# Kernel optimization log

Hardware: AMD Instinct MI355X
Metric: run time of the kernel (lower is better)

The kernel has to match this reference:

```python
import jax, jax.numpy as jnp
import numpy as np
import math

N_CLASSES = 1000
CODE_LENGTH = 1024
IN_FEATURES = 4096
BATCH = 512
MAX_PROB = 0.95
POWER = 1.0


def _hadamard(n):
    # Sylvester construction; n must be a power of 2.
    H = np.array([[1.0]], dtype=np.float64)
    while H.shape[0] < n:
        H = np.block([[H, H], [H, -H]])
    return H


def setup_inputs() -> dict:
    key = jax.random.key(0)
    k1, k2, k3 = jax.random.split(key, 3)
    x = jax.random.normal(k1, (BATCH, IN_FEATURES), dtype=jnp.float32)
    out_feat = CODE_LENGTH - 1  # single head: code_length//1 - 1
    # nn.Linear default init: U(-1/sqrt(fan_in), 1/sqrt(fan_in))
    bound = 1.0 / math.sqrt(IN_FEATURES)
    W = jax.random.uniform(k2, (out_feat, IN_FEATURES), dtype=jnp.float32, minval=-bound, maxval=bound)
    b = jax.random.uniform(k3, (out_feat,), dtype=jnp.float32, minval=-bound, maxval=bound)
    labels = jnp.asarray(_hadamard(CODE_LENGTH)[:N_CLASSES, 1:], dtype=jnp.float32)  # (C, L-1)
    eps = jnp.float32(CODE_LENGTH * math.pow((1.0 - MAX_PROB) / (MAX_PROB * (N_CLASSES - 1)), 1.0 / POWER))
    power = jnp.float32(POWER)
    return {"x": x, "W": W, "b": b, "labels": labels, "eps": eps, "power": power}


def reference(x, W, b, labels, eps, power):
    # Linear head: (B, in) @ (in, L-1) + b
    h = jnp.tanh(x @ W.T + b)                               # (B, L-1)
    # L1 distance to each Hadamard code row: (B, 1, L-1) vs (C, L-1)
    d = jnp.sum(jnp.abs(h[:, None, :] - labels), axis=-1)   # (B, C)
    d = jnp.maximum(d, eps)
    inv = 1.0 / jnp.power(d, power)                          # (B, C)
    return inv / jnp.sum(inv, axis=-1, keepdims=True)
```

## Files before the change

### kernel.cpp

```cpp
#include <hip/hip_runtime.h>

#define BATCH 512
#define INFEAT 4096
#define LOUT 1023
#define NCLS 1000
#define NPAD 1024
#define SPLITK 8

typedef __bf16 bf16x8 __attribute__((ext_vector_type(8)));
typedef float f32x4 __attribute__((ext_vector_type(4)));

__device__ __forceinline__ unsigned short f2bf(float a) {
    unsigned u = __builtin_bit_cast(unsigned, a);
    return (unsigned short)((u + 0x7fffu + ((u >> 16) & 1u)) >> 16);
}
__device__ __forceinline__ unsigned f2bf2(float a, float b) {
    return (unsigned)f2bf(a) | ((unsigned)f2bf(b) << 16);
}
__device__ __forceinline__ float bf2f(unsigned short u) {
    return __builtin_bit_cast(float, ((unsigned)u) << 16);
}

__device__ __forceinline__ void gload_lds16(const void* g, void* l) {
    __builtin_amdgcn_global_load_lds(
        (const __attribute__((address_space(1))) void*)g,
        (__attribute__((address_space(3))) void*)l, 16, 0, 0);
}

__global__ __launch_bounds__(256) void k_cvt(const float* __restrict__ x,
                                             const float* __restrict__ W,
                                             unsigned char* __restrict__ xb,
                                             unsigned char* __restrict__ Wb) {
    int blk = blockIdx.x;
    if (blk < 1024) {
        int g = blk * 256 + threadIdx.x;
        int r = g >> 9, k16 = g & 511;
        const float4* p = (const float4*)(x + (size_t)r * INFEAT + k16 * 8);
        float4 v0 = p[0], v1 = p[1];
        uint4 o;
        o.x = f2bf2(v0.x, v0.y); o.y = f2bf2(v0.z, v0.w);
        o.z = f2bf2(v1.x, v1.y); o.w = f2bf2(v1.z, v1.w);
        *(uint4*)(xb + (size_t)r * 8192 + (k16 >> 3) * 128 + (((k16 & 7) ^ (r & 7)) * 16)) = o;
    } else {
        int g = (blk - 1024) * 256 + threadIdx.x;
        int r = g >> 9, k16 = g & 511;
        uint4 o = {0, 0, 0, 0};
        if (r < LOUT) {
            const float4* p = (const float4*)(W + (size_t)r * INFEAT + k16 * 8);
            float4 v0 = p[0], v1 = p[1];
            o.x = f2bf2(v0.x, v0.y); o.y = f2bf2(v0.z, v0.w);
            o.z = f2bf2(v1.x, v1.y); o.w = f2bf2(v1.z, v1.w);
        }
        *(uint4*)(Wb + (size_t)r * 8192 + (k16 >> 3) * 128 + (((k16 & 7) ^ (r & 7)) * 16)) = o;
    }
}

__global__ __launch_bounds__(256, 2) void k_gemm1(
    const unsigned char* __restrict__ xb, const unsigned char* __restrict__ Wb,
    unsigned short* __restrict__ partial) {
    __shared__ unsigned char lds[49152];
    f32x4 acc[4][2] = {};
    const int bn = blockIdx.x, bm = blockIdx.y, sp = blockIdx.z;
    const int tid = threadIdx.x;
    const int wave = tid >> 6, lane = tid & 63;
    const int lrow = lane & 15, lgrp = lane >> 4;
    const int wr = wave >> 1, wc = wave & 1;
    const int arow0 = bm * 128, brow0 = bn * 64, chunk0 = sp * 8;

    auto STAGE = [&](int bsel, int c) {
        unsigned char* lA = lds + bsel * 24576;
        unsigned char* lB = lA + 16384;
#pragma unroll
        for (int rr = 0; rr < 4; ++rr) {
            int g = rr * 256 + tid;
            int r = g >> 3, s = g & 7;
            gload_lds16(xb + (size_t)(arow0 + r) * 8192 + c * 128 + s * 16,
                        lA + (rr * 256 + wave * 64) * 16);
        }
#pragma unroll
        for (int rr = 0; rr < 2; ++rr) {
            int g = rr * 256 + tid;
            int r = g >> 3, s = g & 7;
            gload_lds16(Wb + (size_t)(brow0 + r) * 8192 + c * 128 + s * 16,
                        lB + (rr * 256 + wave * 64) * 16);
        }
    };

    auto COMPUTE = [&](int bsel) {
        const unsigned char* lA = lds + bsel * 24576;
        const unsigned char* lB = lA + 16384;
#pragma unroll
        for (int ks = 0; ks < 2; ++ks) {
            int swz = ((ks * 4 + lgrp) ^ (lrow & 7)) * 16;
            bf16x8 a[4], b[2];
#pragma unroll
            for (int m = 0; m < 4; ++m)
                a[m] = *(const bf16x8*)(lA + (wr * 64 + m * 16 + lrow) * 128 + swz);
#pragma unroll
            for (int n = 0; n < 2; ++n)
                b[n] = *(const bf16x8*)(lB + (wc * 32 + n * 16 + lrow) * 128 + swz);
#pragma unroll
            for (int m = 0; m < 4; ++m)
#pragma unroll
                for (int n = 0; n < 2; ++n)
                    acc[m][n] = __builtin_amdgcn_mfma_f32_16x16x32_bf16(
                        a[m], b[n], acc[m][n], 0, 0, 0);
        }
    };

    STAGE(0, chunk0);
    asm volatile("s_waitcnt vmcnt(0)" ::: "memory");
    __syncthreads();
#pragma unroll 1
    for (int t = 0; t < 8; ++t) {
        int cur = t & 1;
        if (t + 1 < 8) STAGE(cur ^ 1, chunk0 + t + 1);
        COMPUTE(cur);
        asm volatile("s_waitcnt vmcnt(0)" ::: "memory");
        __syncthreads();
    }

    unsigned short* P = partial + (size_t)sp * (BATCH * NPAD);
#pragma unroll
    for (int m = 0; m < 4; ++m)
#pragma unroll
        for (int n = 0; n < 2; ++n)
#pragma unroll
            for (int reg = 0; reg < 4; ++reg) {
                int r = arow0 + wr * 64 + m * 16 + lgrp * 4 + reg;
                int c = brow0 + wc * 32 + n * 16 + lrow;
                P[(size_t)r * NPAD + c] = f2bf(acc[m][n][reg]);
            }
}

__global__ __launch_bounds__(256) void k_fused(const unsigned short* __restrict__ partial,
                                               const float* __restrict__ bias,
                                               const float* __restrict__ epsp,
                                               const float* __restrict__ powp,
                                               float* __restrict__ out) {
    __shared__ float g[1024];
    __shared__ float wsum[4];
    const int r = blockIdx.x, t = threadIdx.x;
    const int n0 = t * 4;

    f32x4 v = {0.0f, 0.0f, 0.0f, 0.0f};
#pragma unroll
    for (int s = 0; s < SPLITK; ++s) {
        ushort4 p = *(const ushort4*)(partial + ((size_t)s * BATCH + r) * NPAD + n0);
        v[0] += bf2f(p.x); v[1] += bf2f(p.y); v[2] += bf2f(p.z); v[3] += bf2f(p.w);
    }
    float bb[4];
    if (t < 255) {
        float4 b4 = *(const float4*)(bias + n0);
        bb[0] = b4.x; bb[1] = b4.y; bb[2] = b4.z; bb[3] = b4.w;
    } else {
        bb[0] = bias[1020]; bb[1] = bias[1021]; bb[2] = bias[1022]; bb[3] = 0.0f;
    }
    if (t == 0) g[0] = 0.0f;
#pragma unroll
    for (int j = 0; j < 4; ++j) {
        int n = n0 + j;
        if (n < LOUT) g[n + 1] = tanhf(v[j] + bb[j]);
    }
    __syncthreads();

#pragma unroll 1
    for (int s = 0; s < 10; ++s) {
        int st = 1 << s;
#pragma unroll
        for (int pp = 0; pp < 2; ++pp) {
            int p = t + pp * 256;
            int idx = ((p >> s) << (s + 1)) | (p & (st - 1));
            float a = g[idx], c = g[idx + st];
            g[idx] = a + c;
            g[idx + st] = a - c;
        }
        __syncthreads();
    }

    const float eps = *epsp, pw = *powp;
    float iv[4];
    float ss = 0.0f;
#pragma unroll
    for (int j = 0; j < 4; ++j) {
        int c = n0 + j;
        float d = fmaxf(1023.0f - g[c], eps);
        float q = (pw == 1.0f) ? (1.0f / d) : powf(d, -pw);
        if (c >= NCLS) q = 0.0f;
        iv[j] = q;
        ss += q;
    }
#pragma unroll
    for (int m = 32; m; m >>= 1) ss += __shfl_xor(ss, m, 64);
    if ((t & 63) == 0) wsum[t >> 6] = ss;
    __syncthreads();
    float sc = 1.0f / (wsum[0] + wsum[1] + wsum[2] + wsum[3]);

    if (n0 < NCLS) {
        float4 o;
        o.x = iv[0] * sc; o.y = iv[1] * sc; o.z = iv[2] * sc; o.w = iv[3] * sc;
        *(float4*)(out + (size_t)r * NCLS + n0) = o;
    }
}

extern "C" void kernel_launch(void* const* d_in, const int* in_sizes, int n_in,
                              void* d_out, int out_size, void* d_ws, size_t ws_size,
                              hipStream_t stream) {
    const float* x = (const float*)d_in[0];
    const float* W = (const float*)d_in[1];
    const float* b = (const float*)d_in[2];
    const float* epsp = (const float*)d_in[4];
    const float* powp = (const float*)d_in[5];
    float* out = (float*)d_out;

    unsigned char* ws = (unsigned char*)d_ws;
    unsigned char* xb = ws;
    unsigned char* Wb = ws + (4u << 20);
    unsigned short* partial = (unsigned short*)(ws + (12u << 20));

    k_cvt<<<3072, 256, 0, stream>>>(x, W, xb, Wb);
    k_gemm1<<<dim3(16, 4, 8), 256, 0, stream>>>(xb, Wb, partial);
    k_fused<<<512, 256, 0, stream>>>(partial, b, epsp, powp, out);
}
```

Before: 27.93 us.

## Restructure split-K GEMM: stage full A slice in LDS, stream B from global

Replaces the double-buffered 128x64 LDS-tiled GEMM with 1024 blocks, each computing a 64x64 tile over a 512-wide K slice. Each block loads its whole A slice (64 KB) into LDS once, then each wave computes a 16-row strip. B fragments are read directly from global memory into registers with a three-set rotation that prefetches two steps ahead. The aim is more blocks, fewer barriers and less LDS traffic for B. In exchange, B is read redundantly by all four waves, and there is no overlap between the A load and compute.

```diff
diff --git a/kernel.cpp b/kernel.cpp
--- a/kernel.cpp
+++ b/kernel.cpp
@@ -55,82 +55,75 @@
     }
 }
 
-__global__ __launch_bounds__(256, 2) void k_gemm1(
+__global__ __launch_bounds__(256, 2) void k_gemm(
     const unsigned char* __restrict__ xb, const unsigned char* __restrict__ Wb,
     unsigned short* __restrict__ partial) {
-    __shared__ unsigned char lds[49152];
-    f32x4 acc[4][2] = {};
-    const int bn = blockIdx.x, bm = blockIdx.y, sp = blockIdx.z;
+    __shared__ unsigned char lA[65536];
+    const int bid = blockIdx.x;
+    const int work = (bid & 7) * 128 + (bid >> 3);
+    const int sp = work >> 7, rg = (work >> 4) & 7, bn = work & 15;
     const int tid = threadIdx.x;
     const int wave = tid >> 6, lane = tid & 63;
     const int lrow = lane & 15, lgrp = lane >> 4;
-    const int wr = wave >> 1, wc = wave & 1;
-    const int arow0 = bm * 128, brow0 = bn * 64, chunk0 = sp * 8;
-
-    auto STAGE = [&](int bsel, int c) {
-        unsigned char* lA = lds + bsel * 24576;
-        unsigned char* lB = lA + 16384;
-#pragma unroll
-        for (int rr = 0; rr < 4; ++rr) {
-            int g = rr * 256 + tid;
-            int r = g >> 3, s = g & 7;
-            gload_lds16(xb + (size_t)(arow0 + r) * 8192 + c * 128 + s * 16,
-                        lA + (rr * 256 + wave * 64) * 16);
-        }
-#pragma unroll
-        for (int rr = 0; rr < 2; ++rr) {
-            int g = rr * 256 + tid;
-            int r = g >> 3, s = g & 7;
-            gload_lds16(Wb + (size_t)(brow0 + r) * 8192 + c * 128 + s * 16,
-                        lB + (rr * 256 + wave * 64) * 16);
-        }
-    };
-
-    auto COMPUTE = [&](int bsel) {
-        const unsigned char* lA = lds + bsel * 24576;
-        const unsigned char* lB = lA + 16384;
-#pragma unroll
-        for (int ks = 0; ks < 2; ++ks) {
-            int swz = ((ks * 4 + lgrp) ^ (lrow & 7)) * 16;
-            bf16x8 a[4], b[2];
-#pragma unroll
-            for (int m = 0; m < 4; ++m)
-                a[m] = *(const bf16x8*)(lA + (wr * 64 + m * 16 + lrow) * 128 + swz);
-#pragma unroll
-            for (int n = 0; n < 2; ++n)
-                b[n] = *(const bf16x8*)(lB + (wc * 32 + n * 16 + lrow) * 128 + swz);
-#pragma unroll
-            for (int m = 0; m < 4; ++m)
-#pragma unroll
-                for (int n = 0; n < 2; ++n)
-                    acc[m][n] = __builtin_amdgcn_mfma_f32_16x16x32_bf16(
-                        a[m], b[n], acc[m][n], 0, 0, 0);
-        }
-    };
-
-    STAGE(0, chunk0);
+    const int arow0 = rg * 64, brow0 = bn * 64;
+    const int m0 = wave * 16;
+
+#pragma unroll
+    for (int i = 0; i < 16; ++i) {
+        int row = wave * 16 + i;
+        gload_lds16(xb + (size_t)(arow0 + row) * 8192 + sp * 1024 + lane * 16,
+                    lA + row * 1024);
+    }
     asm volatile("s_waitcnt vmcnt(0)" ::: "memory");
     __syncthreads();
-#pragma unroll 1
-    for (int t = 0; t < 8; ++t) {
-        int cur = t & 1;
-        if (t + 1 < 8) STAGE(cur ^ 1, chunk0 + t + 1);
-        COMPUTE(cur);
-        asm volatile("s_waitcnt vmcnt(0)" ::: "memory");
-        __syncthreads();
-    }
+
+    f32x4 acc[4] = {};
+    const int lx = lrow & 7;
+    size_t bbase[4];
+#pragma unroll
+    for (int nf = 0; nf < 4; ++nf)
+        bbase[nf] = (size_t)(brow0 + nf * 16 + lrow) * 8192 + sp * 1024;
+
+    bf16x8 bs0[4], bs1[4], bs2[4];
+
+#define LOADB(KS, SET)                                                        \
+    {                                                                         \
+        _Pragma("unroll")                                                     \
+        for (int nf = 0; nf < 4; ++nf)                                        \
+            SET[nf] = *(const bf16x8*)(Wb + bbase[nf] +                       \
+                                       ((((KS) * 4 + lgrp) ^ lx) * 16));      \
+    }
+#define KS3(KS, CUR, NXT)                                                     \
+    {                                                                         \
+        if ((KS) + 2 < 16) LOADB((KS) + 2, NXT);                              \
+        bf16x8 af = *(const bf16x8*)(lA + (m0 + lrow) * 1024 +                \
+                                     ((((KS) * 4 + lgrp) ^ lx) * 16));        \
+        _Pragma("unroll")                                                     \
+        for (int nf = 0; nf < 4; ++nf)                                        \
+            acc[nf] = __builtin_amdgcn_mfma_f32_16x16x32_bf16(                \
+                af, CUR[nf], acc[nf], 0, 0, 0);                               \
+    }
+
+    LOADB(0, bs0)
+    LOADB(1, bs1)
+    KS3(0, bs0, bs2)  KS3(1, bs1, bs0)  KS3(2, bs2, bs1)
+    KS3(3, bs0, bs2)  KS3(4, bs1, bs0)  KS3(5, bs2, bs1)
+    KS3(6, bs0, bs2)  KS3(7, bs1, bs0)  KS3(8, bs2, bs1)
+    KS3(9, bs0, bs2)  KS3(10, bs1, bs0) KS3(11, bs2, bs1)
+    KS3(12, bs0, bs2) KS3(13, bs1, bs0) KS3(14, bs2, bs1)
+    KS3(15, bs0, bs2)
+#undef KS3
+#undef LOADB
 
     unsigned short* P = partial + (size_t)sp * (BATCH * NPAD);
 #pragma unroll
-    for (int m = 0; m < 4; ++m)
-#pragma unroll
-        for (int n = 0; n < 2; ++n)
-#pragma unroll
-            for (int reg = 0; reg < 4; ++reg) {
-                int r = arow0 + wr * 64 + m * 16 + lgrp * 4 + reg;
-                int c = brow0 + wc * 32 + n * 16 + lrow;
-                P[(size_t)r * NPAD + c] = f2bf(acc[m][n][reg]);
-            }
+    for (int nf = 0; nf < 4; ++nf)
+#pragma unroll
+        for (int reg = 0; reg < 4; ++reg) {
+            int r = arow0 + m0 + lgrp * 4 + reg;
+            int c = brow0 + nf * 16 + lrow;
+            P[(size_t)r * NPAD + c] = f2bf(acc[nf][reg]);
+        }
 }
 
 __global__ __launch_bounds__(256) void k_fused(const unsigned short* __restrict__ partial,
@@ -219,6 +212,6 @@
     unsigned short* partial = (unsigned short*)(ws + (12u << 20));
 
     k_cvt<<<3072, 256, 0, stream>>>(x, W, xb, Wb);
-    k_gemm1<<<dim3(16, 4, 8), 256, 0, stream>>>(xb, Wb, partial);
+    k_gemm<<<1024, 256, 0, stream>>>(xb, Wb, partial);
     k_fused<<<512, 256, 0, stream>>>(partial, b, epsp, powp, out);
 }
```

After: 39.06 us. 1.4x slower.

## Use 128x128 GEMM tiles with split-K 16 and XCD-aware block remap

Applied to the files above, without the earlier changes.

The GEMM tile grows from 128x64 to 128x128 per block, split-K rises from 8 to 16 with 4 K-chunks per block, and blocks are remapped so neighbouring work lands on the same XCD. MFMA sections are wrapped in s_setprio, and __syncthreads becomes a raw s_barrier after an explicit waitcnt. The aim is more data reuse per LDS load and better L2 locality. The cost is twice as many bf16 partial buffers for k_fused to read and reduce, plus higher register and LDS use (64KB per block), which may lower occupancy.

```diff
diff --git a/kernel.cpp b/kernel.cpp
--- a/kernel.cpp
+++ b/kernel.cpp
@@ -5,7 +5,7 @@
 #define LOUT 1023
 #define NCLS 1000
 #define NPAD 1024
-#define SPLITK 8
+#define SPLITK 16
 
 typedef __bf16 bf16x8 __attribute__((ext_vector_type(8)));
 typedef float f32x4 __attribute__((ext_vector_type(4)));
@@ -55,80 +55,80 @@
     }
 }
 
-__global__ __launch_bounds__(256, 2) void k_gemm1(
+__global__ __launch_bounds__(256, 2) void k_gemm(
     const unsigned char* __restrict__ xb, const unsigned char* __restrict__ Wb,
     unsigned short* __restrict__ partial) {
-    __shared__ unsigned char lds[49152];
-    f32x4 acc[4][2] = {};
-    const int bn = blockIdx.x, bm = blockIdx.y, sp = blockIdx.z;
+    __shared__ unsigned char lds[65536];
+    const int bid = blockIdx.x;
+    const int work = (bid & 7) * 64 + (bid >> 3);
+    const int bn = work & 7, bm = (work >> 3) & 3, sp = work >> 5;
     const int tid = threadIdx.x;
     const int wave = tid >> 6, lane = tid & 63;
     const int lrow = lane & 15, lgrp = lane >> 4;
     const int wr = wave >> 1, wc = wave & 1;
-    const int arow0 = bm * 128, brow0 = bn * 64, chunk0 = sp * 8;
+    const int arow0 = bm * 128, brow0 = bn * 128, chunk0 = sp * 4;
+
+    f32x4 acc[4][4] = {};
 
     auto STAGE = [&](int bsel, int c) {
-        unsigned char* lA = lds + bsel * 24576;
+        unsigned char* lA = lds + bsel * 32768;
         unsigned char* lB = lA + 16384;
 #pragma unroll
-        for (int rr = 0; rr < 4; ++rr) {
-            int g = rr * 256 + tid;
+        for (int j = 0; j < 4; ++j) {
+            int g = wave * 256 + j * 64 + lane;
             int r = g >> 3, s = g & 7;
             gload_lds16(xb + (size_t)(arow0 + r) * 8192 + c * 128 + s * 16,
-                        lA + (rr * 256 + wave * 64) * 16);
-        }
-#pragma unroll
-        for (int rr = 0; rr < 2; ++rr) {
-            int g = rr * 256 + tid;
-            int r = g >> 3, s = g & 7;
+                        lA + (wave * 256 + j * 64) * 16);
             gload_lds16(Wb + (size_t)(brow0 + r) * 8192 + c * 128 + s * 16,
-                        lB + (rr * 256 + wave * 64) * 16);
+                        lB + (wave * 256 + j * 64) * 16);
         }
     };
 
     auto COMPUTE = [&](int bsel) {
-        const unsigned char* lA = lds + bsel * 24576;
+        const unsigned char* lA = lds + bsel * 32768;
         const unsigned char* lB = lA + 16384;
 #pragma unroll
         for (int ks = 0; ks < 2; ++ks) {
             int swz = ((ks * 4 + lgrp) ^ (lrow & 7)) * 16;
-            bf16x8 a[4], b[2];
+            bf16x8 fa[4], fb[4];
 #pragma unroll
             for (int m = 0; m < 4; ++m)
-                a[m] = *(const bf16x8*)(lA + (wr * 64 + m * 16 + lrow) * 128 + swz);
-#pragma unroll
-            for (int n = 0; n < 2; ++n)
-                b[n] = *(const bf16x8*)(lB + (wc * 32 + n * 16 + lrow) * 128 + swz);
+                fa[m] = *(const bf16x8*)(lA + (wr * 64 + m * 16 + lrow) * 128 + swz);
+#pragma unroll
+            for (int n = 0; n < 4; ++n)
+                fb[n] = *(const bf16x8*)(lB + (wc * 64 + n * 16 + lrow) * 128 + swz);
+            __builtin_amdgcn_s_setprio(1);
 #pragma unroll
             for (int m = 0; m < 4; ++m)
 #pragma unroll
-                for (int n = 0; n < 2; ++n)
+                for (int n = 0; n < 4; ++n)
                     acc[m][n] = __builtin_amdgcn_mfma_f32_16x16x32_bf16(
-                        a[m], b[n], acc[m][n], 0, 0, 0);
+                        fa[m], fb[n], acc[m][n], 0, 0, 0);
+            __builtin_amdgcn_s_setprio(0);
         }
     };
 
     STAGE(0, chunk0);
     asm volatile("s_waitcnt vmcnt(0)" ::: "memory");
-    __syncthreads();
+    __builtin_amdgcn_s_barrier();
 #pragma unroll 1
-    for (int t = 0; t < 8; ++t) {
-        int cur = t & 1;
-        if (t + 1 < 8) STAGE(cur ^ 1, chunk0 + t + 1);
+    for (int t = 0; t < 4; ++t) {
+        const int cur = t & 1;
+        if (t + 1 < 4) STAGE(cur ^ 1, chunk0 + t + 1);
         COMPUTE(cur);
-        asm volatile("s_waitcnt vmcnt(0)" ::: "memory");
-        __syncthreads();
+        asm volatile("s_waitcnt vmcnt(0) lgkmcnt(0)" ::: "memory");
+        __builtin_amdgcn_s_barrier();
     }
 
     unsigned short* P = partial + (size_t)sp * (BATCH * NPAD);
 #pragma unroll
     for (int m = 0; m < 4; ++m)
 #pragma unroll
-        for (int n = 0; n < 2; ++n)
+        for (int n = 0; n < 4; ++n)
 #pragma unroll
             for (int reg = 0; reg < 4; ++reg) {
                 int r = arow0 + wr * 64 + m * 16 + lgrp * 4 + reg;
-                int c = brow0 + wc * 32 + n * 16 + lrow;
+                int c = brow0 + wc * 64 + n * 16 + lrow;
                 P[(size_t)r * NPAD + c] = f2bf(acc[m][n][reg]);
             }
 }
@@ -219,6 +219,6 @@
     unsigned short* partial = (unsigned short*)(ws + (12u << 20));
 
     k_cvt<<<3072, 256, 0, stream>>>(x, W, xb, Wb);
-    k_gemm1<<<dim3(16, 4, 8), 256, 0, stream>>>(xb, Wb, partial);
+    k_gemm<<<512, 256, 0, stream>>>(xb, Wb, partial);
     k_fused<<<512, 256, 0, stream>>>(partial, b, epsp, powp, out);
 }
```

Result: no change. 28.30 us (+1.3%).
